# Kernel optimization log

Hardware: AMD Instinct MI355X
Metric: run time of the kernel (lower is better)

## Reference

```python
import jax, jax.numpy as jnp
import numpy as np

B, S, DM, H, HD = 2, 2048, 1024, 16, 64
MEM_SIZE = 1000
K_SIMILAR, K_CONTIG = 8, 2
K_TOTAL = K_SIMILAR + K_CONTIG  # 10 memory tokens
NEG = -1e9


def setup_inputs() -> dict:
    key = jax.random.key(0)
    k1, k2, k3, k4, k5, k6 = jax.random.split(key, 6)
    inputs = jax.random.normal(k1, (B, S, DM), dtype=jnp.float32)
    attention_mask = jnp.ones((B, S), dtype=jnp.float32)
    Wq = jax.random.normal(k2, (DM, H * HD), dtype=jnp.float32) * 0.02
    Wk = jax.random.normal(k3, (DM, H * HD), dtype=jnp.float32) * 0.02
    Wv = jax.random.normal(k4, (DM, H * HD), dtype=jnp.float32) * 0.02
    Wo = jax.random.normal(k5, (H * HD, DM), dtype=jnp.float32) * 0.02
    events = jax.random.normal(k6, (MEM_SIZE, H * HD), dtype=jnp.float32) * 0.02
    return {"inputs": inputs, "attention_mask": attention_mask,
            "Wq": Wq, "Wk": Wk, "Wv": Wv, "Wo": Wo, "events": events}


def _forward(inputs, attention_mask, Wq, Wk, Wv, Wo, events):
    # projections (no bias), split heads: [B, H, S, HD]
    q = (inputs @ Wq).reshape(B, S, H, HD).transpose(0, 2, 1, 3)
    k = (inputs @ Wk).reshape(B, S, H, HD).transpose(0, 2, 1, 3)
    v = (inputs @ Wv).reshape(B, S, H, HD).transpose(0, 2, 1, 3)

    # --- episodic retrieval: cosine top-k of last-token key vs events ---
    qvec = k[:, :, -1, :].reshape(B, H * HD)                       # [B, D]
    qn = qvec / (jnp.linalg.norm(qvec, axis=-1, keepdims=True) + 1e-8)
    en = events / (jnp.linalg.norm(events, axis=-1, keepdims=True) + 1e-8)
    sims = qn @ en.T                                               # [B, M]
    _, topk_idx = jax.lax.top_k(sims, K_TOTAL)                     # [B, K]
    retrieved = events[topk_idx]                                   # [B, K, D]
    retrieved_k = retrieved.reshape(B, K_TOTAL, H, HD).transpose(0, 2, 1, 3)  # [B,H,K,HD]
    retrieved_v = retrieved_k                                      # non-differential path

    aug_k = jnp.concatenate([retrieved_k, k], axis=2)              # [B,H,K+S,HD]
    aug_v = jnp.concatenate([retrieved_v, v], axis=2)

    # --- ALiBi bias: slopes * (pos_i - pos_j) on original cols, 0 on memory cols ---
    slopes = 2.0 ** (-8.0 * jnp.arange(1, H + 1, dtype=jnp.float32) / H)  # [H]
    positions = jnp.arange(S, dtype=jnp.float32)
    pos_diff = positions[:, None] - positions[None, :]             # [S, S]
    alibi = slopes[:, None, None] * pos_diff                       # [H, S, S]
    alibi = jnp.concatenate([jnp.zeros((H, S, K_TOTAL), jnp.float32), alibi], axis=-1)

    # --- causal mask: -1e9 strictly-upper on original cols, 0 on memory cols ---
    tri = jnp.where(jnp.arange(S)[None, :] > jnp.arange(S)[:, None], NEG, 0.0)  # [S,S]
    causal = jnp.concatenate([jnp.zeros((S, K_TOTAL), jnp.float32), tri], axis=-1)

    # --- padding mask: memory tokens always attendable ---
    aug_mask = jnp.concatenate([jnp.ones((B, K_TOTAL), jnp.float32), attention_mask], axis=-1)
    mask_bias = (1.0 - aug_mask)[:, None, None, :] * NEG           # [B,1,1,K+S]

    scores = jnp.einsum("bhqd,bhkd->bhqk", q, aug_k) / np.sqrt(HD)
    scores = scores + alibi[None] + causal[None, None] + mask_bias
    attn = jax.nn.softmax(scores, axis=-1)
    out = jnp.einsum("bhqk,bhkd->bhqd", attn, aug_v)               # [B,H,S,HD]
    out = out.transpose(0, 2, 1, 3).reshape(B, S, H * HD)
    return out @ Wo


def reference(inputs, attention_mask, Wq, Wk, Wv, Wo, events):
    return _forward(inputs, attention_mask, Wq, Wk, Wv, Wo, events)
```

## Files before the change

### kernel.cpp

```cpp
#include <hip/hip_runtime.h>
#include <hip/hip_bf16.h>
#include <math.h>

#define B_   2
#define S_   2048
#define DM_  1024
#define H_   16
#define HD_  64
#define MEM_ 1000
#define KTOT 10
#define NROW (B_ * S_)
#define NEG9 (-1e9f)
#define LDK  72
#define NITEMS 1024

typedef __attribute__((ext_vector_type(8))) short short8;
typedef __attribute__((ext_vector_type(4))) float f32x4;

__device__ __forceinline__ void gll16(const __hip_bfloat16* g, __hip_bfloat16* l) {
    __builtin_amdgcn_global_load_lds(
        (const __attribute__((address_space(1))) void*)g,
        (__attribute__((address_space(3))) void*)l, 16, 0, 0);
}

__global__ __launch_bounds__(256) void prep(const float* __restrict__ inputs,
                                            const float* __restrict__ Wq,
                                            const float* __restrict__ Wk,
                                            const float* __restrict__ Wv,
                                            const float* __restrict__ Wo,
                                            __hip_bfloat16* __restrict__ Ax,
                                            __hip_bfloat16* __restrict__ Wt,
                                            float* __restrict__ lk,
                                            int* __restrict__ ctr) {
    const int bx = blockIdx.x, tid = threadIdx.x;
    if (bx == 0 && tid == 0) *ctr = 0;

    if (bx < 2048) {
        const size_t i = ((size_t)bx * 256 + tid) * 8;
        float4 a = *(const float4*)&inputs[i];
        float4 b = *(const float4*)&inputs[i + 4];
        alignas(16) __hip_bfloat16 t[8];
        t[0] = __float2bfloat16(a.x); t[1] = __float2bfloat16(a.y);
        t[2] = __float2bfloat16(a.z); t[3] = __float2bfloat16(a.w);
        t[4] = __float2bfloat16(b.x); t[5] = __float2bfloat16(b.y);
        t[6] = __float2bfloat16(b.z); t[7] = __float2bfloat16(b.w);
        *(short8*)&Ax[i] = *(short8*)t;
        return;
    }
    if (bx < 3072) {
        const int idx = bx - 2048;
        const int g = idx >> 8, rem = idx & 255;
        const float* W = (g == 0) ? Wq : (g == 1) ? Wk : (g == 2) ? Wv : Wo;
        const int n0 = (rem & 15) * 64, k0 = (rem >> 4) * 64;
        __shared__ float T[64][65];
        {
            const int r = tid >> 4, c4 = (tid & 15) * 4;
#pragma unroll
            for (int p = 0; p < 4; ++p) {
                float4 v = *(const float4*)&W[(size_t)(k0 + r + p * 16) * 1024 + n0 + c4];
                T[r + p * 16][c4 + 0] = v.x; T[r + p * 16][c4 + 1] = v.y;
                T[r + p * 16][c4 + 2] = v.z; T[r + p * 16][c4 + 3] = v.w;
            }
        }
        __syncthreads();
        {
            const int n = tid >> 3, off = (tid & 7) * 8;
#pragma unroll
            for (int p = 0; p < 2; ++p) {
                const int nn = n + p * 32;
                alignas(16) __hip_bfloat16 t[8];
#pragma unroll
                for (int j = 0; j < 8; ++j) t[j] = __float2bfloat16(T[off + j][nn]);
                *(short8*)&Wt[((size_t)(g * 1024 + n0 + nn)) * 1024 + k0 + off] = *(short8*)t;
            }
        }
        return;
    }
    {
        const int idx = bx - 3072;
        const int xblk = idx & 15, b = idx >> 4;
        const int cl = tid & 63;
        const int col = xblk * 64 + cl;
        const int kq = tid >> 6;
        __shared__ float xr[1024];
        __shared__ float part[4][64];
        for (int i = tid; i < 1024; i += 256)
            xr[i] = inputs[((size_t)(b * S_ + S_ - 1)) * 1024 + i];
        __syncthreads();
        float acc = 0.f;
#pragma unroll 4
        for (int k = kq * 256; k < kq * 256 + 256; ++k)
            acc += xr[k] * Wk[(size_t)k * 1024 + col];
        part[kq][cl] = acc;
        __syncthreads();
        if (tid < 64)
            lk[b * 1024 + xblk * 64 + tid] =
                part[0][tid] + part[1][tid] + part[2][tid] + part[3][tid];
    }
}

__device__ __forceinline__ void store_out(__hip_bfloat16* p, float x) { *p = __float2bfloat16(x); }
__device__ __forceinline__ void store_out(float* p, float x) { *p = x; }

template <typename OutT>
__global__ __launch_bounds__(256) void gemm_mfma(const __hip_bfloat16* __restrict__ A,
                                                 const __hip_bfloat16* __restrict__ Bt,
                                                 OutT* __restrict__ C, int ldc) {
    __shared__ __hip_bfloat16 As[128 * 32];
    __shared__ __hip_bfloat16 Bs[128 * 32];
    const int tid = threadIdx.x;
    const int wave = tid >> 6, lane = tid & 63;
    const int quad = lane >> 4, lm = lane & 15;
    const int wr = wave >> 1, wc = wave & 1;
    const int m0 = blockIdx.y * 128, n0 = blockIdx.x * 128;

    const int r0 = tid >> 2, c0 = (tid & 3) * 8;
    const __hip_bfloat16* ga0 = &A[(size_t)(m0 + r0) * 1024 + c0];
    const __hip_bfloat16* ga1 = &A[(size_t)(m0 + 64 + r0) * 1024 + c0];
    const __hip_bfloat16* gb0 = &Bt[(size_t)(n0 + r0) * 1024 + c0];
    const __hip_bfloat16* gb1 = &Bt[(size_t)(n0 + 64 + r0) * 1024 + c0];
    __hip_bfloat16* la0 = &As[(wave * 64) * 8];
    __hip_bfloat16* la1 = &As[(256 + wave * 64) * 8];
    __hip_bfloat16* lb0 = &Bs[(wave * 64) * 8];
    __hip_bfloat16* lb1 = &Bs[(256 + wave * 64) * 8];

    f32x4 acc[4][4];
#pragma unroll
    for (int i = 0; i < 4; ++i)
#pragma unroll
        for (int j = 0; j < 4; ++j) acc[i][j] = (f32x4){0.f, 0.f, 0.f, 0.f};

    for (int k0 = 0; k0 < 1024; k0 += 32) {
        __syncthreads();
        gll16(ga0 + k0, la0);
        gll16(ga1 + k0, la1);
        gll16(gb0 + k0, lb0);
        gll16(gb1 + k0, lb1);
        __syncthreads();
        short8 af[4], bf4[4];
#pragma unroll
        for (int mt = 0; mt < 4; ++mt)
            af[mt] = *(const short8*)&As[(wr * 64 + mt * 16 + lm) * 32 + quad * 8];
#pragma unroll
        for (int nt = 0; nt < 4; ++nt)
            bf4[nt] = *(const short8*)&Bs[(wc * 64 + nt * 16 + lm) * 32 + quad * 8];
#pragma unroll
        for (int mt = 0; mt < 4; ++mt)
#pragma unroll
            for (int nt = 0; nt < 4; ++nt)
                acc[mt][nt] = __builtin_amdgcn_mfma_f32_16x16x32_bf16(
                    af[mt], bf4[nt], acc[mt][nt], 0, 0, 0);
    }
#pragma unroll
    for (int mt = 0; mt < 4; ++mt)
#pragma unroll
        for (int nt = 0; nt < 4; ++nt) {
            const int col = n0 + wc * 64 + nt * 16 + lm;
#pragma unroll
            for (int i = 0; i < 4; ++i) {
                const int row = m0 + wr * 64 + mt * 16 + quad * 4 + i;
                store_out(&C[(size_t)row * ldc + col], acc[mt][nt][i]);
            }
        }
}

template <typename OutT>
__global__ __launch_bounds__(256) void gemm_mfma64(const __hip_bfloat16* __restrict__ A,
                                                   const __hip_bfloat16* __restrict__ Bt,
                                                   OutT* __restrict__ C, int ldc) {
    __shared__ __hip_bfloat16 As[64 * 32];
    __shared__ __hip_bfloat16 Bs[128 * 32];
    const int tid = threadIdx.x;
    const int wave = tid >> 6, lane = tid & 63;
    const int quad = lane >> 4, lm = lane & 15;
    const int wr = wave >> 1, wc = wave & 1;
    const int m0 = blockIdx.y * 64, n0 = blockIdx.x * 128;

    const int r0 = tid >> 2, c0 = (tid & 3) * 8;
    const __hip_bfloat16* ga  = &A[(size_t)(m0 + r0) * 1024 + c0];
    const __hip_bfloat16* gb0 = &Bt[(size_t)(n0 + r0) * 1024 + c0];
    const __hip_bfloat16* gb1 = &Bt[(size_t)(n0 + 64 + r0) * 1024 + c0];
    __hip_bfloat16* la  = &As[(wave * 64) * 8];
    __hip_bfloat16* lb0 = &Bs[(wave * 64) * 8];
    __hip_bfloat16* lb1 = &Bs[(256 + wave * 64) * 8];

    f32x4 acc[2][4];
#pragma unroll
    for (int i = 0; i < 2; ++i)
#pragma unroll
        for (int j = 0; j < 4; ++j) acc[i][j] = (f32x4){0.f, 0.f, 0.f, 0.f};

    for (int k0 = 0; k0 < 1024; k0 += 32) {
        __syncthreads();
        gll16(ga + k0, la);
        gll16(gb0 + k0, lb0);
        gll16(gb1 + k0, lb1);
        __syncthreads();
        short8 af[2], bf4[4];
#pragma unroll
        for (int mt = 0; mt < 2; ++mt)
            af[mt] = *(const short8*)&As[(wr * 32 + mt * 16 + lm) * 32 + quad * 8];
#pragma unroll
        for (int nt = 0; nt < 4; ++nt)
            bf4[nt] = *(const short8*)&Bs[(wc * 64 + nt * 16 + lm) * 32 + quad * 8];
#pragma unroll
        for (int mt = 0; mt < 2; ++mt)
#pragma unroll
            for (int nt = 0; nt < 4; ++nt)
                acc[mt][nt] = __builtin_amdgcn_mfma_f32_16x16x32_bf16(
                    af[mt], bf4[nt], acc[mt][nt], 0, 0, 0);
    }
#pragma unroll
    for (int mt = 0; mt < 2; ++mt)
#pragma unroll
        for (int nt = 0; nt < 4; ++nt) {
            const int col = n0 + wc * 64 + nt * 16 + lm;
#pragma unroll
            for (int i = 0; i < 4; ++i) {
                const int row = m0 + wr * 32 + mt * 16 + quad * 4 + i;
                store_out(&C[(size_t)row * ldc + col], acc[mt][nt][i]);
            }
        }
}

__global__ __launch_bounds__(256) void sims_kernel(const float* __restrict__ lk,
                                                   const float* __restrict__ events,
                                                   float* __restrict__ sims) {
    const int b = blockIdx.y;
    const int tid = threadIdx.x;
    const int wave = tid >> 6, lane = tid & 63;
    __shared__ float qv[1024];
    for (int i = tid; i < 1024; i += 256)
        qv[i] = lk[b * 1024 + i];
    __syncthreads();

    const int m = blockIdx.x * 4 + wave;
    if (m >= MEM_) return;
    const float* ev = &events[(size_t)m * 1024];
    float dot = 0.f, nrm = 0.f;
    for (int d = lane; d < 1024; d += 64) {
        float e = ev[d];
        dot += qv[d] * e;
        nrm += e * e;
    }
    for (int off = 32; off; off >>= 1) {
        dot += __shfl_down(dot, off);
        nrm += __shfl_down(nrm, off);
    }
    if (lane == 0) sims[b * 1024 + m] = dot / (sqrtf(nrm) + 1e-8f);
}

__global__ __launch_bounds__(64) void topk10_kernel(const float* __restrict__ sims,
                                                    int* __restrict__ topk) {
    const int b = blockIdx.x;
    const int lane = threadIdx.x;
    const int base = lane * 16;
    float v[16];
#pragma unroll
    for (int j = 0; j < 16; ++j) {
        const int m = base + j;
        v[j] = (m < MEM_) ? sims[b * 1024 + m] : -INFINITY;
    }
    for (int it = 0; it < KTOT; ++it) {
        float best = -INFINITY; int bi = 0x7fffffff;
#pragma unroll
        for (int j = 0; j < 16; ++j)
            if (v[j] > best) { best = v[j]; bi = base + j; }
        for (int off = 32; off; off >>= 1) {
            const float ob = __shfl_xor(best, off);
            const int   oi = __shfl_xor(bi, off);
            if (ob > best || (ob == best && oi < bi)) { best = ob; bi = oi; }
        }
        if (lane == 0) topk[b * KTOT + it] = bi;
#pragma unroll
        for (int j = 0; j < 16; ++j)
            if (base + j == bi) v[j] = -INFINITY;
    }
}

__global__ __launch_bounds__(256) void attn_mfma(
        const __hip_bfloat16* __restrict__ qkv,
        const float* __restrict__ events,
        const int* __restrict__ topk,
        const float* __restrict__ amask,
        __hip_bfloat16* __restrict__ out,
        int* __restrict__ ctr) {
    const int tid = threadIdx.x;
    const int wave = tid >> 6, lane = tid & 63;
    const int quad = lane >> 4, lm = lane & 15;

    const __hip_bfloat16* qf = qkv;
    const __hip_bfloat16* kf = qkv + 1024;
    const __hip_bfloat16* vf = qkv + 2048;

    __shared__ __hip_bfloat16 Ks[2][64 * LDK];
    __shared__ __hip_bfloat16 Vt[2][80 * LDK];
    __shared__ __hip_bfloat16 Ps[64 * LDK];
    __shared__ float colb[2][64];
    __shared__ float redb[4];
    __shared__ int sItem;

    const int va = tid & 31, vdc = tid >> 5;
    const int vtok0 = va * 2, vd0 = vdc * 8;

    for (int i = tid * 8; i < 64 * LDK; i += 256 * 8) {
        *(int4*)&Vt[0][i] = make_int4(0, 0, 0, 0);
        *(int4*)&Vt[1][i] = make_int4(0, 0, 0, 0);
    }
    for (int i = tid; i < 16 * LDK; i += 256) {
        const int r = i / LDK;
        const __hip_bfloat16 v = __float2bfloat16(r == 0 ? 1.0f : 0.0f);
        Vt[0][64 * LDK + i] = v;
        Vt[1][64 * LDK + i] = v;
    }

    for (;;) {
        __syncthreads();
        if (tid == 0) sItem = atomicAdd(ctr, 1);
        __syncthreads();
        const int n = sItem;
        if (n >= NITEMS) break;

        const int qt = 31 - (n >> 5);
        const int q0 = qt * 64;
        const int inner = n & 31;
        const int h = 15 - ((inner >> 1) & 15);
        const int b = inner & 1;
        const float slope = exp2f(-0.5f * (float)(h + 1));

        short8 pk[2], pv0, pv1;
        float pam = 1.f;
        auto prefetchKV = [&](int kt) {
            const __hip_bfloat16* ks = &kf[((size_t)(b * S_ + kt * 64)) * 3072 + h * 64];
#pragma unroll
            for (int u = 0; u < 2; ++u) {
                int c = tid * 2 + u, row = c >> 3, off = (c & 7) * 8;
                pk[u] = *(const short8*)&ks[(size_t)row * 3072 + off];
            }
            const __hip_bfloat16* v0 =
                &vf[((size_t)(b * S_ + kt * 64 + vtok0)) * 3072 + h * 64 + vd0];
            pv0 = *(const short8*)v0;
            pv1 = *(const short8*)(v0 + 3072);
            if (tid < 64) pam = amask[b * S_ + kt * 64 + tid];
        };
        auto stageKV = [&](int kt, int pb) {
#pragma unroll
            for (int u = 0; u < 2; ++u) {
                int c = tid * 2 + u, row = c >> 3, off = (c & 7) * 8;
                *(short8*)&Ks[pb][row * LDK + off] = pk[u];
            }
#pragma unroll
            for (int j = 0; j < 8; ++j) {
                short2 pr; pr.x = pv0[j]; pr.y = pv1[j];
                *(short2*)&Vt[pb][(vd0 + j) * LDK + vtok0] = pr;
            }
            if (tid < 64)
                colb[pb][tid] = fmaf(-slope, (float)(kt * 64 + tid), (1.f - pam) * NEG9);
        };

        prefetchKV(0);

        short8 qa[2];
        {
            const __hip_bfloat16* qsrc =
                &qf[((size_t)(b * S_ + q0 + wave * 16 + lm)) * 3072 + h * 64 + quad * 8];
            qa[0] = *(const short8*)qsrc;
            qa[1] = *(const short8*)(qsrc + 32);
        }
        if (tid < 80) {
            const int tok = tid >> 3, d0 = (tid & 7) * 8;
            const int ev = topk[b * KTOT + tok];
            const float* es = &events[(size_t)ev * 1024 + h * 64 + d0];
#pragma unroll
            for (int j = 0; j < 8; ++j) {
                __hip_bfloat16 x = __float2bfloat16(es[j]);
                Ks[0][tok * LDK + d0 + j] = x;
                Vt[0][(d0 + j) * LDK + tok] = x;
            }
        }
        __syncthreads();

        float m_[4], mshift[4];
        f32x4 Oa[5];
#pragma unroll
        for (int i = 0; i < 4; ++i) {
            m_[i] = -INFINITY;
            mshift[i] = -slope * (float)(q0 + wave * 16 + quad * 4 + i);
        }
#pragma unroll
        for (int nt = 0; nt < 5; ++nt) Oa[nt] = (f32x4){0.f, 0.f, 0.f, 0.f};

        auto qk = [&](f32x4* sa, const __hip_bfloat16* Kp) {
#pragma unroll
            for (int nt = 0; nt < 4; ++nt) sa[nt] = (f32x4){0.f, 0.f, 0.f, 0.f};
#pragma unroll
            for (int ks2 = 0; ks2 < 2; ++ks2) {
#pragma unroll
                for (int nt = 0; nt < 4; ++nt) {
                    short8 bk = *(const short8*)&Kp[(nt * 16 + lm) * LDK + ks2 * 32 + quad * 8];
                    sa[nt] = __builtin_amdgcn_mfma_f32_16x16x32_bf16(qa[ks2], bk, sa[nt], 0, 0, 0);
                }
            }
        };
        auto pv = [&](const __hip_bfloat16* Vp) {
#pragma unroll
            for (int ks2 = 0; ks2 < 2; ++ks2) {
                short8 ap = *(const short8*)&Ps[(wave * 16 + lm) * LDK + ks2 * 32 + quad * 8];
#pragma unroll
                for (int nt = 0; nt < 5; ++nt) {
                    short8 bv = *(const short8*)&Vp[(nt * 16 + lm) * LDK + ks2 * 32 + quad * 8];
                    Oa[nt] = __builtin_amdgcn_mfma_f32_16x16x32_bf16(ap, bv, Oa[nt], 0, 0, 0);
                }
            }
        };

        auto softmax_online = [&](const f32x4* sa, int kt, bool diag, const float* cbp) {
            float cb[4];
            if (kt >= 0) {
#pragma unroll
                for (int nt = 0; nt < 4; ++nt) cb[nt] = cbp[nt * 16 + lm];
            }
#pragma unroll
            for (int i = 0; i < 4; ++i) {
                const int lr = wave * 16 + quad * 4 + i;
                const int rg = q0 + lr;
                float s[4];
#pragma unroll
                for (int nt = 0; nt < 4; ++nt) {
                    const int cc = nt * 16 + lm;
                    if (kt < 0) {
                        s[nt] = (cc < KTOT) ? fmaf(sa[nt][i], 0.125f, mshift[i]) : NEG9;
                    } else {
                        float v = fmaf(sa[nt][i], 0.125f, cb[nt]);
                        s[nt] = (diag && kt * 64 + cc > rg) ? NEG9 : v;
                    }
                }
                float rmax = fmaxf(fmaxf(s[0], s[1]), fmaxf(s[2], s[3]));
#pragma unroll
                for (int off = 1; off < 16; off <<= 1)
                    rmax = fmaxf(rmax, __shfl_xor(rmax, off, 16));
                const float newm = fmaxf(m_[i], rmax);
                const float al = __expf(m_[i] - newm);
                m_[i] = newm;
#pragma unroll
                for (int nt = 0; nt < 4; ++nt)
                    Ps[lr * LDK + nt * 16 + lm] = __float2bfloat16(__expf(s[nt] - newm));
#pragma unroll
                for (int nt = 0; nt < 5; ++nt)
                    Oa[nt][i] *= al;
            }
        };

        auto softmax_fast = [&](const f32x4* sa, int cbase, bool diag, const float* cbp) {
            float cb[4];
#pragma unroll
            for (int nt = 0; nt < 4; ++nt) cb[nt] = cbp[nt * 16 + lm];
#pragma unroll
            for (int i = 0; i < 4; ++i) {
                const int lr = wave * 16 + quad * 4 + i;
                const float cm = m_[i];
                float p[4];
#pragma unroll
                for (int nt = 0; nt < 4; ++nt)
                    p[nt] = __expf(fmaf(sa[nt][i], 0.125f, cb[nt]) - cm);
                if (diag) {
                    const int rg = q0 + lr;
#pragma unroll
                    for (int nt = 0; nt < 4; ++nt)
                        if (cbase + nt * 16 + lm > rg) p[nt] = 0.f;
                }
#pragma unroll
                for (int nt = 0; nt < 4; ++nt)
                    Ps[lr * LDK + nt * 16 + lm] = __float2bfloat16(p[nt]);
            }
        };

        {
            f32x4 sa[4];
            qk(sa, Ks[0]);
            softmax_online(sa, -1, false, nullptr);
            pv(Vt[0]);
        }
        stageKV(0, 1);
        if (qt >= 1) prefetchKV(1);
        __syncthreads();

        {
            f32x4 sa[4];
            qk(sa, Ks[1]);
            softmax_online(sa, 0, qt == 0, colb[1]);
            pv(Vt[1]);
        }
        {
            float mloc = fminf(fminf(m_[0], m_[1]), fminf(m_[2], m_[3]));
#pragma unroll
            for (int off = 1; off < 64; off <<= 1)
                mloc = fminf(mloc, __shfl_xor(mloc, off, 64));
            if (lane == 0) redb[wave] = mloc;
        }
        if (qt >= 1) stageKV(1, 0);
        if (qt >= 2) prefetchKV(2);
        __syncthreads();

        int ktend = 0;
        if (qt >= 1) {
            const float mmin = fminf(fminf(redb[0], redb[1]), fminf(redb[2], redb[3]));
            ktend = min(qt, (int)((118.f - mmin) / (64.f * slope)));
        }
        for (int kt = 1; kt <= ktend; ++kt) {
            const int pb = (kt + 1) & 1;
            f32x4 sa[4];
            qk(sa, Ks[pb]);
            softmax_fast(sa, kt * 64, kt == qt, colb[pb]);
            pv(Vt[pb]);
            if (kt < ktend) stageKV(kt + 1, kt & 1);
            if (kt + 1 < ktend) prefetchKV(kt + 2);
            __syncthreads();
        }

#pragma unroll
        for (int i = 0; i < 4; ++i) {
            const int lr = wave * 16 + quad * 4 + i;
            const float l = __shfl(Oa[4][i], (lane & 48));
            const float inv = 1.f / l;
            __hip_bfloat16* dst = &out[((size_t)(b * S_ + q0 + lr)) * 1024 + h * 64 + lm];
#pragma unroll
            for (int nt = 0; nt < 4; ++nt)
                dst[nt * 16] = __float2bfloat16(Oa[nt][i] * inv);
        }
    }
}

extern "C" void kernel_launch(void* const* d_in, const int* in_sizes, int n_in,
                              void* d_out, int out_size, void* d_ws, size_t ws_size,
                              hipStream_t stream) {
    const float* inputs = (const float*)d_in[0];
    const float* amask  = (const float*)d_in[1];
    const float* Wq     = (const float*)d_in[2];
    const float* Wk     = (const float*)d_in[3];
    const float* Wv     = (const float*)d_in[4];
    const float* Wo     = (const float*)d_in[5];
    const float* events = (const float*)d_in[6];
    float* out = (float*)d_out;

    __hip_bfloat16* Ax  = (__hip_bfloat16*)d_ws;
    __hip_bfloat16* Wt  = Ax + (size_t)NROW * 1024;
    __hip_bfloat16* qkv = Wt + (size_t)4096 * 1024;
    __hip_bfloat16* ao  = qkv + (size_t)NROW * 3072;
    float* lk   = (float*)(ao + (size_t)NROW * 1024);
    float* sims = lk + 2 * 1024;
    int* topk   = (int*)(sims + 2 * 1024);
    int* ctr    = topk + B_ * KTOT;

    dim3 blk(256);
    prep<<<3104, blk, 0, stream>>>(inputs, Wq, Wk, Wv, Wo, Ax, Wt, lk, ctr);
    sims_kernel<<<dim3(250, B_), blk, 0, stream>>>(lk, events, sims);
    topk10_kernel<<<B_, 64, 0, stream>>>(sims, topk);
    gemm_mfma<__hip_bfloat16><<<dim3(24, 32), blk, 0, stream>>>(Ax, Wt, qkv, 3072);
    attn_mfma<<<768, blk, 0, stream>>>(qkv, events, topk, amask, ao, ctr);
    gemm_mfma64<float><<<dim3(8, 64), blk, 0, stream>>>(
        ao, Wt + (size_t)3072 * 1024, out, 1024);
}
```

Measured before the change: 227.4 us.

## Split attention KV range across two wave-pairs with split-softmax merge

Restructures the attention kernel so that each block's 4 waves form two halves. Each half processes a different part of the key range: one half takes the memory tile plus the low tiles, the other takes the tiles from the midpoint up to the diagonal. Each wave now handles 32 query rows (two MFMA row tiles), so K/V fragments are reused across more rows. The two partial results are merged through LDS using the max/sum softmax combine. The kernel also switches to exp2 with a pre-folded log2e scale and adjusts the ALiBi early-cutoff threshold. The persistent grid is reduced from 768 to 512 blocks. Register pressure rises, and the extra merge step plus uneven split work may offset the shorter serial KV loop.

```diff
diff --git a/kernel.cpp b/kernel.cpp
--- a/kernel.cpp
+++ b/kernel.cpp
@@ -13,9 +13,14 @@
 #define NEG9 (-1e9f)
 #define LDK  72
 #define NITEMS 1024
+#define SC_  0.18033688f
+#define TH_  170.238f
 
 typedef __attribute__((ext_vector_type(8))) short short8;
+typedef __attribute__((ext_vector_type(4))) short s16x4;
 typedef __attribute__((ext_vector_type(4))) float f32x4;
+
+__device__ __forceinline__ float __exp2(float x) { return __builtin_amdgcn_exp2f(x); }
 
 __device__ __forceinline__ void gll16(const __hip_bfloat16* g, __hip_bfloat16* l) {
     __builtin_amdgcn_global_load_lds(
@@ -288,31 +293,31 @@
     const int tid = threadIdx.x;
     const int wave = tid >> 6, lane = tid & 63;
     const int quad = lane >> 4, lm = lane & 15;
+    const int ha = wave >> 1;
+    const int wp = wave & 1;
+    const int htid = tid & 127;
 
     const __hip_bfloat16* qf = qkv;
     const __hip_bfloat16* kf = qkv + 1024;
     const __hip_bfloat16* vf = qkv + 2048;
 
-    __shared__ __hip_bfloat16 Ks[2][64 * LDK];
-    __shared__ __hip_bfloat16 Vt[2][80 * LDK];
-    __shared__ __hip_bfloat16 Ps[64 * LDK];
-    __shared__ float colb[2][64];
+    __shared__ __hip_bfloat16 Ks2[2][64 * LDK];
+    __shared__ __hip_bfloat16 Vt2[2][64 * LDK];
+    __shared__ __hip_bfloat16 Ones[16 * LDK];
+    __shared__ __hip_bfloat16 Ps2[2][64 * LDK];
+    __shared__ float colb2[2][64];
     __shared__ float redb[4];
     __shared__ int sItem;
 
-    const int va = tid & 31, vdc = tid >> 5;
-    const int vtok0 = va * 2, vd0 = vdc * 8;
+    const int krow = htid >> 1, koff = (htid & 1) * 32;
+    const int vtok0 = (htid & 15) * 4, vd0 = (htid >> 4) * 8;
 
     for (int i = tid * 8; i < 64 * LDK; i += 256 * 8) {
-        *(int4*)&Vt[0][i] = make_int4(0, 0, 0, 0);
-        *(int4*)&Vt[1][i] = make_int4(0, 0, 0, 0);
-    }
-    for (int i = tid; i < 16 * LDK; i += 256) {
-        const int r = i / LDK;
-        const __hip_bfloat16 v = __float2bfloat16(r == 0 ? 1.0f : 0.0f);
-        Vt[0][64 * LDK + i] = v;
-        Vt[1][64 * LDK + i] = v;
-    }
+        *(int4*)&Vt2[0][i] = make_int4(0, 0, 0, 0);
+        *(int4*)&Vt2[1][i] = make_int4(0, 0, 0, 0);
+    }
+    for (int i = tid; i < 16 * LDK; i += 256)
+        Ones[i] = __float2bfloat16(i < LDK ? 1.0f : 0.0f);
 
     for (;;) {
         __syncthreads();
@@ -326,47 +331,57 @@
         const int inner = n & 31;
         const int h = 15 - ((inner >> 1) & 15);
         const int b = inner & 1;
-        const float slope = exp2f(-0.5f * (float)(h + 1));
-
-        short8 pk[2], pv0, pv1;
+        const float slope2 = __exp2(-0.5f * (float)(h + 1)) * 1.44269504f;
+        const int mid = (qt + 1) >> 1;
+
+        short8 pk[4], pv4[4];
         float pam = 1.f;
         auto prefetchKV = [&](int kt) {
-            const __hip_bfloat16* ks = &kf[((size_t)(b * S_ + kt * 64)) * 3072 + h * 64];
-#pragma unroll
-            for (int u = 0; u < 2; ++u) {
-                int c = tid * 2 + u, row = c >> 3, off = (c & 7) * 8;
-                pk[u] = *(const short8*)&ks[(size_t)row * 3072 + off];
-            }
+            const __hip_bfloat16* ks =
+                &kf[((size_t)(b * S_ + kt * 64 + krow)) * 3072 + h * 64 + koff];
+#pragma unroll
+            for (int u = 0; u < 4; ++u) pk[u] = *(const short8*)&ks[u * 8];
             const __hip_bfloat16* v0 =
                 &vf[((size_t)(b * S_ + kt * 64 + vtok0)) * 3072 + h * 64 + vd0];
-            pv0 = *(const short8*)v0;
-            pv1 = *(const short8*)(v0 + 3072);
-            if (tid < 64) pam = amask[b * S_ + kt * 64 + tid];
+#pragma unroll
+            for (int t = 0; t < 4; ++t) pv4[t] = *(const short8*)&v0[(size_t)t * 3072];
+            if (htid < 64) pam = amask[b * S_ + kt * 64 + htid];
         };
-        auto stageKV = [&](int kt, int pb) {
-#pragma unroll
-            for (int u = 0; u < 2; ++u) {
-                int c = tid * 2 + u, row = c >> 3, off = (c & 7) * 8;
-                *(short8*)&Ks[pb][row * LDK + off] = pk[u];
-            }
+        auto stageKV = [&](int kt) {
+#pragma unroll
+            for (int u = 0; u < 4; ++u)
+                *(short8*)&Ks2[ha][krow * LDK + koff + u * 8] = pk[u];
 #pragma unroll
             for (int j = 0; j < 8; ++j) {
-                short2 pr; pr.x = pv0[j]; pr.y = pv1[j];
-                *(short2*)&Vt[pb][(vd0 + j) * LDK + vtok0] = pr;
-            }
-            if (tid < 64)
-                colb[pb][tid] = fmaf(-slope, (float)(kt * 64 + tid), (1.f - pam) * NEG9);
+                s16x4 w;
+                w[0] = pv4[0][j]; w[1] = pv4[1][j]; w[2] = pv4[2][j]; w[3] = pv4[3][j];
+                *(s16x4*)&Vt2[ha][(vd0 + j) * LDK + vtok0] = w;
+            }
+            if (htid < 64)
+                colb2[ha][htid] = fmaf(-slope2, (float)(kt * 64 + htid), (1.f - pam) * NEG9);
         };
 
-        prefetchKV(0);
-
-        short8 qa[2];
-        {
+        short8 qa[2][2];
+#pragma unroll
+        for (int mt = 0; mt < 2; ++mt) {
             const __hip_bfloat16* qsrc =
-                &qf[((size_t)(b * S_ + q0 + wave * 16 + lm)) * 3072 + h * 64 + quad * 8];
-            qa[0] = *(const short8*)qsrc;
-            qa[1] = *(const short8*)(qsrc + 32);
-        }
+                &qf[((size_t)(b * S_ + q0 + wp * 32 + mt * 16 + lm)) * 3072 + h * 64 + quad * 8];
+            qa[mt][0] = *(const short8*)qsrc;
+            qa[mt][1] = *(const short8*)(qsrc + 32);
+        }
+        float m_[2][4], mshift[2][4];
+        f32x4 Oa[2][5];
+#pragma unroll
+        for (int mt = 0; mt < 2; ++mt)
+#pragma unroll
+            for (int i = 0; i < 4; ++i) {
+                m_[mt][i] = -INFINITY;
+                mshift[mt][i] = -slope2 * (float)(q0 + wp * 32 + mt * 16 + quad * 4 + i);
+                Oa[mt][i] = (f32x4){0.f, 0.f, 0.f, 0.f};
+            }
+        Oa[0][4] = (f32x4){0.f, 0.f, 0.f, 0.f};
+        Oa[1][4] = (f32x4){0.f, 0.f, 0.f, 0.f};
+
         if (tid < 80) {
             const int tok = tid >> 3, d0 = (tid & 7) * 8;
             const int ev = topk[b * KTOT + tok];
@@ -374,159 +389,187 @@
 #pragma unroll
             for (int j = 0; j < 8; ++j) {
                 __hip_bfloat16 x = __float2bfloat16(es[j]);
-                Ks[0][tok * LDK + d0 + j] = x;
-                Vt[0][(d0 + j) * LDK + tok] = x;
-            }
-        }
-        __syncthreads();
-
-        float m_[4], mshift[4];
-        f32x4 Oa[5];
-#pragma unroll
-        for (int i = 0; i < 4; ++i) {
-            m_[i] = -INFINITY;
-            mshift[i] = -slope * (float)(q0 + wave * 16 + quad * 4 + i);
-        }
-#pragma unroll
-        for (int nt = 0; nt < 5; ++nt) Oa[nt] = (f32x4){0.f, 0.f, 0.f, 0.f};
-
-        auto qk = [&](f32x4* sa, const __hip_bfloat16* Kp) {
-#pragma unroll
-            for (int nt = 0; nt < 4; ++nt) sa[nt] = (f32x4){0.f, 0.f, 0.f, 0.f};
-#pragma unroll
-            for (int ks2 = 0; ks2 < 2; ++ks2) {
+                Ks2[0][tok * LDK + d0 + j] = x;
+                Vt2[0][(d0 + j) * LDK + tok] = x;
+            }
+        }
+        if (ha == 0) { if (mid > 0) prefetchKV(0); }
+        else prefetchKV(mid);
+
+        auto computeTile = [&](bool memt, bool online, bool diag, int cbase) {
+            f32x4 sa[2][4];
+            const __hip_bfloat16* Kp = Ks2[ha];
+#pragma unroll
+            for (int mt = 0; mt < 2; ++mt)
+#pragma unroll
+                for (int nt = 0; nt < 4; ++nt) sa[mt][nt] = (f32x4){0.f, 0.f, 0.f, 0.f};
+#pragma unroll
+            for (int ks2 = 0; ks2 < 2; ++ks2)
 #pragma unroll
                 for (int nt = 0; nt < 4; ++nt) {
                     short8 bk = *(const short8*)&Kp[(nt * 16 + lm) * LDK + ks2 * 32 + quad * 8];
-                    sa[nt] = __builtin_amdgcn_mfma_f32_16x16x32_bf16(qa[ks2], bk, sa[nt], 0, 0, 0);
+#pragma unroll
+                    for (int mt = 0; mt < 2; ++mt)
+                        sa[mt][nt] = __builtin_amdgcn_mfma_f32_16x16x32_bf16(
+                            qa[mt][ks2], bk, sa[mt][nt], 0, 0, 0);
                 }
+            float cb[4];
+            if (!memt) {
+#pragma unroll
+                for (int nt = 0; nt < 4; ++nt) cb[nt] = colb2[ha][nt * 16 + lm];
+            }
+#pragma unroll
+            for (int mt = 0; mt < 2; ++mt)
+#pragma unroll
+                for (int i = 0; i < 4; ++i) {
+                    const int lr = wp * 32 + mt * 16 + quad * 4 + i;
+                    const int rg = q0 + lr;
+                    float s[4];
+#pragma unroll
+                    for (int nt = 0; nt < 4; ++nt) {
+                        const int cc = nt * 16 + lm;
+                        float v;
+                        if (memt)
+                            v = (cc < KTOT) ? fmaf(sa[mt][nt][i], SC_, mshift[mt][i]) : NEG9;
+                        else {
+                            v = fmaf(sa[mt][nt][i], SC_, cb[nt]);
+                            if (diag && cbase + cc > rg) v = NEG9;
+                        }
+                        s[nt] = v;
+                    }
+                    float cm;
+                    if (online) {
+                        float rmax = fmaxf(fmaxf(s[0], s[1]), fmaxf(s[2], s[3]));
+#pragma unroll
+                        for (int off = 1; off < 16; off <<= 1)
+                            rmax = fmaxf(rmax, __shfl_xor(rmax, off, 16));
+                        const float newm = fmaxf(m_[mt][i], rmax);
+                        const float al = __exp2(m_[mt][i] - newm);
+                        m_[mt][i] = newm; cm = newm;
+#pragma unroll
+                        for (int nt = 0; nt < 5; ++nt) Oa[mt][nt][i] *= al;
+                    } else cm = m_[mt][i];
+#pragma unroll
+                    for (int nt = 0; nt < 4; ++nt)
+                        Ps2[ha][lr * LDK + nt * 16 + lm] = __float2bfloat16(__exp2(s[nt] - cm));
+                }
+#pragma unroll
+            for (int ks2 = 0; ks2 < 2; ++ks2) {
+                short8 ap0 = *(const short8*)&Ps2[ha][(wp * 32 + lm) * LDK + ks2 * 32 + quad * 8];
+                short8 ap1 = *(const short8*)&Ps2[ha][(wp * 32 + 16 + lm) * LDK + ks2 * 32 + quad * 8];
+#pragma unroll
+                for (int nt = 0; nt < 4; ++nt) {
+                    short8 bv = *(const short8*)&Vt2[ha][(nt * 16 + lm) * LDK + ks2 * 32 + quad * 8];
+                    Oa[0][nt] = __builtin_amdgcn_mfma_f32_16x16x32_bf16(ap0, bv, Oa[0][nt], 0, 0, 0);
+                    Oa[1][nt] = __builtin_amdgcn_mfma_f32_16x16x32_bf16(ap1, bv, Oa[1][nt], 0, 0, 0);
+                }
+                short8 bvO = *(const short8*)&Ones[lm * LDK + ks2 * 32 + quad * 8];
+                Oa[0][4] = __builtin_amdgcn_mfma_f32_16x16x32_bf16(ap0, bvO, Oa[0][4], 0, 0, 0);
+                Oa[1][4] = __builtin_amdgcn_mfma_f32_16x16x32_bf16(ap1, bvO, Oa[1][4], 0, 0, 0);
             }
         };
-        auto pv = [&](const __hip_bfloat16* Vp) {
-#pragma unroll
-            for (int ks2 = 0; ks2 < 2; ++ks2) {
-                short8 ap = *(const short8*)&Ps[(wave * 16 + lm) * LDK + ks2 * 32 + quad * 8];
-#pragma unroll
-                for (int nt = 0; nt < 5; ++nt) {
-                    short8 bv = *(const short8*)&Vp[(nt * 16 + lm) * LDK + ks2 * 32 + quad * 8];
-                    Oa[nt] = __builtin_amdgcn_mfma_f32_16x16x32_bf16(ap, bv, Oa[nt], 0, 0, 0);
-                }
-            }
-        };
-
-        auto softmax_online = [&](const f32x4* sa, int kt, bool diag, const float* cbp) {
-            float cb[4];
-            if (kt >= 0) {
-#pragma unroll
-                for (int nt = 0; nt < 4; ++nt) cb[nt] = cbp[nt * 16 + lm];
-            }
-#pragma unroll
-            for (int i = 0; i < 4; ++i) {
-                const int lr = wave * 16 + quad * 4 + i;
-                const int rg = q0 + lr;
-                float s[4];
-#pragma unroll
-                for (int nt = 0; nt < 4; ++nt) {
-                    const int cc = nt * 16 + lm;
-                    if (kt < 0) {
-                        s[nt] = (cc < KTOT) ? fmaf(sa[nt][i], 0.125f, mshift[i]) : NEG9;
-                    } else {
-                        float v = fmaf(sa[nt][i], 0.125f, cb[nt]);
-                        s[nt] = (diag && kt * 64 + cc > rg) ? NEG9 : v;
-                    }
-                }
-                float rmax = fmaxf(fmaxf(s[0], s[1]), fmaxf(s[2], s[3]));
-#pragma unroll
-                for (int off = 1; off < 16; off <<= 1)
-                    rmax = fmaxf(rmax, __shfl_xor(rmax, off, 16));
-                const float newm = fmaxf(m_[i], rmax);
-                const float al = __expf(m_[i] - newm);
-                m_[i] = newm;
-#pragma unroll
-                for (int nt = 0; nt < 4; ++nt)
-                    Ps[lr * LDK + nt * 16 + lm] = __float2bfloat16(__expf(s[nt] - newm));
-#pragma unroll
-                for (int nt = 0; nt < 5; ++nt)
-                    Oa[nt][i] *= al;
-            }
-        };
-
-        auto softmax_fast = [&](const f32x4* sa, int cbase, bool diag, const float* cbp) {
-            float cb[4];
-#pragma unroll
-            for (int nt = 0; nt < 4; ++nt) cb[nt] = cbp[nt * 16 + lm];
-#pragma unroll
-            for (int i = 0; i < 4; ++i) {
-                const int lr = wave * 16 + quad * 4 + i;
-                const float cm = m_[i];
-                float p[4];
-#pragma unroll
-                for (int nt = 0; nt < 4; ++nt)
-                    p[nt] = __expf(fmaf(sa[nt][i], 0.125f, cb[nt]) - cm);
-                if (diag) {
-                    const int rg = q0 + lr;
-#pragma unroll
-                    for (int nt = 0; nt < 4; ++nt)
-                        if (cbase + nt * 16 + lm > rg) p[nt] = 0.f;
-                }
-#pragma unroll
-                for (int nt = 0; nt < 4; ++nt)
-                    Ps[lr * LDK + nt * 16 + lm] = __float2bfloat16(p[nt]);
-            }
-        };
-
-        {
-            f32x4 sa[4];
-            qk(sa, Ks[0]);
-            softmax_online(sa, -1, false, nullptr);
-            pv(Vt[0]);
-        }
-        stageKV(0, 1);
-        if (qt >= 1) prefetchKV(1);
-        __syncthreads();
-
-        {
-            f32x4 sa[4];
-            qk(sa, Ks[1]);
-            softmax_online(sa, 0, qt == 0, colb[1]);
-            pv(Vt[1]);
-        }
-        {
-            float mloc = fminf(fminf(m_[0], m_[1]), fminf(m_[2], m_[3]));
+        auto redbWrite = [&]() {
+            float mloc = fminf(fminf(m_[0][0], m_[0][1]), fminf(m_[0][2], m_[0][3]));
+            mloc = fminf(mloc, fminf(fminf(m_[1][0], m_[1][1]), fminf(m_[1][2], m_[1][3])));
 #pragma unroll
             for (int off = 1; off < 64; off <<= 1)
                 mloc = fminf(mloc, __shfl_xor(mloc, off, 64));
             if (lane == 0) redb[wave] = mloc;
-        }
-        if (qt >= 1) stageKV(1, 0);
-        if (qt >= 2) prefetchKV(2);
-        __syncthreads();
-
-        int ktend = 0;
-        if (qt >= 1) {
-            const float mmin = fminf(fminf(redb[0], redb[1]), fminf(redb[2], redb[3]));
-            ktend = min(qt, (int)((118.f - mmin) / (64.f * slope)));
-        }
-        for (int kt = 1; kt <= ktend; ++kt) {
-            const int pb = (kt + 1) & 1;
-            f32x4 sa[4];
-            qk(sa, Ks[pb]);
-            softmax_fast(sa, kt * 64, kt == qt, colb[pb]);
-            pv(Vt[pb]);
-            if (kt < ktend) stageKV(kt + 1, kt & 1);
-            if (kt + 1 < ktend) prefetchKV(kt + 2);
+        };
+
+        if (ha == 1) {
+            stageKV(mid);
+            if (mid + 1 <= qt) prefetchKV(mid + 1);
+        }
+        __syncthreads();
+        if (ha == 0) {
+            computeTile(true, true, false, 0);
+        } else {
+            computeTile(false, true, mid == qt, mid * 64);
+            redbWrite();
+        }
+
+        __syncthreads();
+        const int kendB = max(mid, min(qt,
+            (int)((TH_ - fminf(redb[2], redb[3])) / (64.f * slope2))));
+        if (ha == 0) {
+            if (mid > 0) { stageKV(0); if (1 <= mid - 1) prefetchKV(1); }
+        } else {
+            if (mid + 1 <= kendB) stageKV(mid + 1);
+            if (mid + 2 <= kendB) prefetchKV(mid + 2);
+        }
+        __syncthreads();
+        if (ha == 0) {
+            if (mid > 0) { computeTile(false, true, false, 0); redbWrite(); }
+        } else if (mid + 1 <= kendB) {
+            computeTile(false, false, (mid + 1) == qt, (mid + 1) * 64);
+        }
+
+        int kendA = -1, smax = 2;
+        for (int s = 2;; ++s) {
             __syncthreads();
-        }
-
-#pragma unroll
-        for (int i = 0; i < 4; ++i) {
-            const int lr = wave * 16 + quad * 4 + i;
-            const float l = __shfl(Oa[4][i], (lane & 48));
-            const float inv = 1.f / l;
-            __hip_bfloat16* dst = &out[((size_t)(b * S_ + q0 + lr)) * 1024 + h * 64 + lm];
-#pragma unroll
-            for (int nt = 0; nt < 4; ++nt)
-                dst[nt * 16] = __float2bfloat16(Oa[nt][i] * inv);
+            if (s == 2) {
+                if (mid > 0)
+                    kendA = min(mid - 1, max(0,
+                        (int)((TH_ - fminf(redb[0], redb[1])) / (64.f * slope2))));
+                smax = max(kendA + 2, kendB - mid + 1);
+            }
+            if (s >= smax) break;
+            if (ha == 0) {
+                if (s - 1 <= kendA) stageKV(s - 1);
+                if (s <= kendA) prefetchKV(s);
+            } else {
+                if (mid + s <= kendB) stageKV(mid + s);
+                if (mid + s + 1 <= kendB) prefetchKV(mid + s + 1);
+            }
+            __syncthreads();
+            if (ha == 0) {
+                if (s - 1 <= kendA) computeTile(false, false, false, (s - 1) * 64);
+            } else if (mid + s <= kendB) {
+                computeTile(false, false, (mid + s) == qt, (mid + s) * 64);
+            }
+        }
+
+        float l_[2][4];
+#pragma unroll
+        for (int mt = 0; mt < 2; ++mt)
+#pragma unroll
+            for (int i = 0; i < 4; ++i) l_[mt][i] = __shfl(Oa[mt][4][i], (lane & 48));
+
+        float* mO = (float*)Ks2;
+        float* mM = colb2[0];
+        float* mL = colb2[1];
+        if (ha == 1) {
+#pragma unroll
+            for (int mt = 0; mt < 2; ++mt)
+#pragma unroll
+                for (int i = 0; i < 4; ++i) {
+                    const int lr = wp * 32 + mt * 16 + quad * 4 + i;
+#pragma unroll
+                    for (int nt = 0; nt < 4; ++nt)
+                        mO[lr * 64 + nt * 16 + lm] = Oa[mt][nt][i];
+                    if (lm == 0) { mM[lr] = m_[mt][i]; mL[lr] = l_[mt][i]; }
+                }
+        }
+        __syncthreads();
+        if (ha == 0) {
+#pragma unroll
+            for (int mt = 0; mt < 2; ++mt)
+#pragma unroll
+                for (int i = 0; i < 4; ++i) {
+                    const int lr = wp * 32 + mt * 16 + quad * 4 + i;
+                    const float mB = mM[lr], lB = mL[lr];
+                    const float mA = m_[mt][i], lA = l_[mt][i];
+                    const float mm = fmaxf(mA, mB);
+                    const float fA = __exp2(mA - mm), fB = __exp2(mB - mm);
+                    const float inv = 1.f / (lA * fA + lB * fB);
+                    __hip_bfloat16* dst =
+                        &out[((size_t)(b * S_ + q0 + lr)) * 1024 + h * 64 + lm];
+#pragma unroll
+                    for (int nt = 0; nt < 4; ++nt)
+                        dst[nt * 16] = __float2bfloat16(
+                            (Oa[mt][nt][i] * fA + mO[lr * 64 + nt * 16 + lm] * fB) * inv);
+                }
         }
     }
 }
@@ -557,7 +600,7 @@
     sims_kernel<<<dim3(250, B_), blk, 0, stream>>>(lk, events, sims);
     topk10_kernel<<<B_, 64, 0, stream>>>(sims, topk);
     gemm_mfma<__hip_bfloat16><<<dim3(24, 32), blk, 0, stream>>>(Ax, Wt, qkv, 3072);
-    attn_mfma<<<768, blk, 0, stream>>>(qkv, events, topk, amask, ao, ctr);
+    attn_mfma<<<512, blk, 0, stream>>>(qkv, events, topk, amask, ao, ctr);
     gemm_mfma64<float><<<dim3(8, 64), blk, 0, stream>>>(
         ao, Wt + (size_t)3072 * 1024, out, 1024);
 }
```

Measured after the change: 272.6 us. 19.9% more time.
